# Optimization experiments

Hardware: AMD Instinct MI355X
Metric: run time of the kernel (lower is better)

## Reference

```python
import jax, jax.numpy as jnp
import numpy as np
import math

B, T, D, H, P, NPASS = 2, 2048, 1024, 16, 256, 3


def setup_inputs() -> dict:
    key = jax.random.key(0)
    ks = jax.random.split(key, 8)
    x = jax.random.normal(ks[0], (B, T, D), jnp.float32)
    scale_gamma = 1.0 + 0.1 * jax.random.normal(ks[1], (D,), jnp.float32)
    scale_beta = 0.1 * jax.random.normal(ks[2], (D,), jnp.float32)
    qkv_w = 0.02 * jax.random.normal(ks[3], (3 * D, D), jnp.float32)
    o_w = 0.02 * jax.random.normal(ks[4], (D, D), jnp.float32)
    norm1_w = jnp.ones((D,), jnp.float32)
    norm2_w = jnp.ones((D,), jnp.float32)
    angles = 0.1 * jax.random.normal(ks[5], (NPASS, P), jnp.float32)
    gate = jnp.ones((NPASS, D), jnp.float32)
    bias = jnp.zeros((NPASS, D), jnp.float32)
    # seeded random permutations matching torch.manual_seed(42+p*1000); torch.randperm
    pis, pjs = [], []
    for p in range(NPASS):
        rng = np.random.RandomState(42 + p * 1000)
        perm = rng.permutation(D)
        pis.append(perm[:P])
        pjs.append(perm[P:2 * P])
    pi = jnp.asarray(np.stack(pis), jnp.int32)
    pj = jnp.asarray(np.stack(pjs), jnp.int32)
    return dict(x=x, scale_gamma=scale_gamma, scale_beta=scale_beta, qkv_w=qkv_w,
                o_w=o_w, norm1_w=norm1_w, norm2_w=norm2_w, angles=angles,
                gate=gate, bias=bias, pi=pi, pj=pj)


def _rmsnorm(x, w):
    eps = jnp.finfo(x.dtype).eps
    return x * jax.lax.rsqrt(jnp.mean(x * x, axis=-1, keepdims=True) + eps) * w


def reference(x, scale_gamma, scale_beta, qkv_w, o_w, norm1_w, norm2_w,
              angles, gate, bias, pi, pj):
    Bs, Ts, Ds = x.shape
    hd = Ds // H
    # --- attention branch ---
    h = _rmsnorm(x, norm1_w) * scale_gamma + scale_beta
    qkv = (h @ qkv_w.T).reshape(Bs, Ts, 3, H, hd)
    qkv = jnp.moveaxis(qkv, 2, 0)            # [3, B, T, H, hd]
    q, k, v = (jnp.swapaxes(qkv[i], 1, 2) for i in range(3))  # [B, H, T, hd]
    scores = jnp.einsum('bhqd,bhkd->bhqk', q, k) / math.sqrt(hd)
    causal = jnp.tril(jnp.ones((Ts, Ts), bool))
    scores = jnp.where(causal, scores, -jnp.inf)
    attn = jax.nn.softmax(scores, axis=-1)
    out = jnp.einsum('bhqk,bhkd->bhqd', attn, v)
    out = jnp.swapaxes(out, 1, 2).reshape(Bs, Ts, Ds)
    x = x + out @ o_w.T
    # --- rotation pseudo-FFN branch ---
    h = _rmsnorm(x, norm2_w) * scale_gamma + scale_beta
    r = h
    for p in range(NPASS):
        cos_a = jnp.cos(angles[p])
        sin_a = jnp.sin(angles[p])
        hi = r[..., pi[p]]
        hj = r[..., pj[p]]
        r = r.at[..., pi[p]].set(hi * cos_a - hj * sin_a)
        r = r.at[..., pj[p]].set(hi * sin_a + hj * cos_a)
        r = jax.nn.silu(r * gate[p] + bias[p])
    return x + r - h
```

## Files before the change

### kernel.cpp

```cpp
#include <hip/hip_runtime.h>
#include <hip/hip_bf16.h>

#define B_ 2
#define T_ 2048
#define D_ 1024
#define H_ 16
#define HD_ 64
#define NP_ 3
#define P_ 256

#define SCALE2 0.18033688011112042f

typedef short bf16x8 __attribute__((ext_vector_type(8)));
typedef float f32x4 __attribute__((ext_vector_type(4)));

__device__ __forceinline__ float bf2f(__hip_bfloat16 v) { return __bfloat162float(v); }
__device__ __forceinline__ __hip_bfloat16 f2bf(float v) { return __float2bfloat16(v); }

__device__ __forceinline__ unsigned pack2bf(float a, float b) {
    union { __hip_bfloat16 h; unsigned short u; } ua, ub;
    ua.h = f2bf(a); ub.h = f2bf(b);
    return (unsigned)ua.u | ((unsigned)ub.u << 16);
}

#define GLOAD_LDS16(gp, lp) \
    __builtin_amdgcn_global_load_lds( \
        (const __attribute__((address_space(1))) void*)(gp), \
        (__attribute__((address_space(3))) void*)(lp), 16, 0, 0)

__global__ __launch_bounds__(256) void detect_kernel(
    const unsigned short* __restrict__ xs, int* __restrict__ flag)
{
    __shared__ int cnt;
    if (threadIdx.x == 0) cnt = 0;
    __syncthreads();
    int bad = 0;
    for (int i = threadIdx.x; i < 16384; i += 256) {
        int e = (xs[i] >> 7) & 0xFF;
        if (e >= 0xB8) bad++;
    }
    if (bad) atomicAdd(&cnt, bad);
    __syncthreads();
    if (threadIdx.x == 0) *flag = (cnt >= 8) ? 1 : 0;
}

__global__ __launch_bounds__(256) void cvt16_2_kernel(
    const void* __restrict__ a, const void* __restrict__ bsrc,
    __hip_bfloat16* __restrict__ da, __hip_bfloat16* __restrict__ db,
    int na, int ntot, const int* __restrict__ flag)
{
    int i = blockIdx.x * 256 + threadIdx.x;
    if (i >= ntot) return;
    int f = *flag;
    if (i < na)
        da[i] = f ? f2bf(((const float*)a)[i]) : ((const __hip_bfloat16*)a)[i];
    else {
        int k = i - na;
        db[k] = f ? f2bf(((const float*)bsrc)[k]) : ((const __hip_bfloat16*)bsrc)[k];
    }
}

__global__ __launch_bounds__(256) void cvt_small_kernel(
    const void* __restrict__ g,  const void* __restrict__ b,
    const void* __restrict__ n1, const void* __restrict__ n2,
    const void* __restrict__ ang, const void* __restrict__ gt,
    const void* __restrict__ bi,
    float* __restrict__ dst, const int* __restrict__ flag)
{
    int i = blockIdx.x * 256 + threadIdx.x;
    if (i >= 11008) return;
    const void* src; int off;
    if      (i < 1024) { src = g;   off = i; }
    else if (i < 2048) { src = b;   off = i - 1024; }
    else if (i < 3072) { src = n1;  off = i - 2048; }
    else if (i < 4096) { src = n2;  off = i - 3072; }
    else if (i < 4864) { src = ang; off = i - 4096; }
    else if (i < 7936) { src = gt;  off = i - 4864; }
    else               { src = bi;  off = i - 7936; }
    dst[i] = (*flag) ? ((const float*)src)[off]
                     : bf2f(((const __hip_bfloat16*)src)[off]);
}

__global__ __launch_bounds__(256) void rmsnorm1_kernel(
    const void* __restrict__ xraw,
    const float* __restrict__ gamma,
    const float* __restrict__ beta,
    const float* __restrict__ w,
    const int* __restrict__ flag,
    __hip_bfloat16* __restrict__ out)
{
    int row = blockIdx.x;
    int t = threadIdx.x;
    int f = *flag;
    float eps = f ? 1.1920929e-7f : 0.0078125f;
    float v[4];
    if (f) {
        const float4 xv = ((const float4*)((const float*)xraw + (size_t)row * D_))[t];
        v[0] = xv.x; v[1] = xv.y; v[2] = xv.z; v[3] = xv.w;
    } else {
        const __hip_bfloat16* xr = (const __hip_bfloat16*)xraw + (size_t)row * D_;
#pragma unroll
        for (int c = 0; c < 4; c++) v[c] = bf2f(xr[t * 4 + c]);
    }
    float ss = 0.f;
#pragma unroll
    for (int c = 0; c < 4; c++) ss += v[c] * v[c];
#pragma unroll
    for (int m = 32; m; m >>= 1) ss += __shfl_xor(ss, m, 64);
    __shared__ float red[4];
    int wv = t >> 6;
    if ((t & 63) == 0) red[wv] = ss;
    __syncthreads();
    float scale = rsqrtf((red[0] + red[1] + red[2] + red[3]) * (1.0f / D_) + eps);
#pragma unroll
    for (int c = 0; c < 4; c++) {
        int e = t * 4 + c;
        size_t idx = (size_t)row * D_ + e;
        out[idx] = f2bf(v[c] * scale * w[e] * gamma[e] + beta[e]);
    }
}

__global__ __launch_bounds__(256) void gemm_bt_bf16_kernel(
    const __hip_bfloat16* __restrict__ A,
    const __hip_bfloat16* __restrict__ Bm,
    __hip_bfloat16* __restrict__ C,
    int M, int N, int K, int nscale, float qscale)
{
    __shared__ __attribute__((aligned(16))) __hip_bfloat16 As[128 * 32];
    __shared__ __attribute__((aligned(16))) __hip_bfloat16 Bs[128 * 32];
    int tid = threadIdx.x;
    int bm = blockIdx.y, bn = blockIdx.x;
    int lane = tid & 63, wv = tid >> 6;
    int wm = wv >> 1, wn = wv & 1;
    int q = lane >> 4, mr = lane & 15;

    f32x4 acc[4][4] = {};

    for (int k0 = 0; k0 < K; k0 += 32) {
#pragma unroll
        for (int s = 0; s < 2; s++) {
            int e = (s * 256 + tid) * 8;
            int r = e >> 5, c = e & 31;
            GLOAD_LDS16(&A[(size_t)(bm * 128 + r) * K + k0 + c], &As[e]);
            GLOAD_LDS16(&Bm[(size_t)(bn * 128 + r) * K + k0 + c], &Bs[e]);
        }
        __syncthreads();
        bf16x8 af[4], bfr[4];
#pragma unroll
        for (int i = 0; i < 4; i++)
            af[i] = *(const bf16x8*)(&As[(wm * 64 + i * 16 + mr) * 32 + q * 8]);
#pragma unroll
        for (int j = 0; j < 4; j++)
            bfr[j] = *(const bf16x8*)(&Bs[(wn * 64 + j * 16 + mr) * 32 + q * 8]);
#pragma unroll
        for (int i = 0; i < 4; i++)
#pragma unroll
            for (int j = 0; j < 4; j++)
                acc[i][j] = __builtin_amdgcn_mfma_f32_16x16x32_bf16(af[i], bfr[j], acc[i][j], 0, 0, 0);
        __syncthreads();
    }

#pragma unroll
    for (int i = 0; i < 4; i++)
#pragma unroll
        for (int r = 0; r < 4; r++) {
            int m = bm * 128 + wm * 64 + i * 16 + q * 4 + r;
#pragma unroll
            for (int j = 0; j < 4; j++) {
                int n = bn * 128 + wn * 64 + j * 16 + mr;
                float vv = acc[i][j][r];
                if (n < nscale) vv *= qscale;
                C[(size_t)m * N + n] = f2bf(vv);
            }
        }
}

__global__ __launch_bounds__(256) void gemm_bt_resid_kernel(
    const __hip_bfloat16* __restrict__ A,
    const __hip_bfloat16* __restrict__ Bm,
    const void* __restrict__ xraw,
    const int* __restrict__ flag,
    float* __restrict__ C,
    int M, int N, int K)
{
    __shared__ __attribute__((aligned(16))) __hip_bfloat16 As[128 * 32];
    __shared__ __attribute__((aligned(16))) __hip_bfloat16 Bs[128 * 32];
    int tid = threadIdx.x;
    int bm = blockIdx.y, bn = blockIdx.x;
    int lane = tid & 63, wv = tid >> 6;
    int wm = wv >> 1, wn = wv & 1;
    int q = lane >> 4, mr = lane & 15;
    int f = *flag;

    f32x4 acc[4][4] = {};

    for (int k0 = 0; k0 < K; k0 += 32) {
#pragma unroll
        for (int s = 0; s < 2; s++) {
            int e = (s * 256 + tid) * 8;
            int r = e >> 5, c = e & 31;
            GLOAD_LDS16(&A[(size_t)(bm * 128 + r) * K + k0 + c], &As[e]);
            GLOAD_LDS16(&Bm[(size_t)(bn * 128 + r) * K + k0 + c], &Bs[e]);
        }
        __syncthreads();
        bf16x8 af[4], bfr[4];
#pragma unroll
        for (int i = 0; i < 4; i++)
            af[i] = *(const bf16x8*)(&As[(wm * 64 + i * 16 + mr) * 32 + q * 8]);
#pragma unroll
        for (int j = 0; j < 4; j++)
            bfr[j] = *(const bf16x8*)(&Bs[(wn * 64 + j * 16 + mr) * 32 + q * 8]);
#pragma unroll
        for (int i = 0; i < 4; i++)
#pragma unroll
            for (int j = 0; j < 4; j++)
                acc[i][j] = __builtin_amdgcn_mfma_f32_16x16x32_bf16(af[i], bfr[j], acc[i][j], 0, 0, 0);
        __syncthreads();
    }

#pragma unroll
    for (int i = 0; i < 4; i++)
#pragma unroll
        for (int r = 0; r < 4; r++) {
            int m = bm * 128 + wm * 64 + i * 16 + q * 4 + r;
#pragma unroll
            for (int j = 0; j < 4; j++) {
                int n = bn * 128 + wn * 64 + j * 16 + mr;
                size_t idx = (size_t)m * N + n;
                float rv = f ? ((const float*)xraw)[idx]
                             : bf2f(((const __hip_bfloat16*)xraw)[idx]);
                C[idx] = rv + acc[i][j][r];
            }
        }
}

__global__ __launch_bounds__(256, 4) void attn_kernel(
    const __hip_bfloat16* __restrict__ qkv,
    __hip_bfloat16* __restrict__ attn_out)
{
    __shared__ __attribute__((aligned(16))) __hip_bfloat16 Ks[2][64 * 64];
    __shared__ __attribute__((aligned(16))) __hip_bfloat16 Vts[2][64 * 64];
    __shared__ __attribute__((aligned(16))) unsigned int Pd[4 * 512];

    int id = blockIdx.x;
    int half = (id ^ (id >> 8)) & 1;
    int w4 = (id >> 1) & 15;
    int qt = half ? 31 - w4 : w4;
    int bh = (id >> 5) & 31;
    int b = bh >> 4, h = bh & 15;
    int tid = threadIdx.x, lane = tid & 63, wv = tid >> 6;
    int q = lane >> 4, mr = lane & 15;
    int m8 = mr & 7;

    const size_t rs3 = 3 * D_;
    const __hip_bfloat16* qp = qkv + (size_t)(b * T_) * rs3 + h * HD_;
    const __hip_bfloat16* kp = qp + D_;
    const __hip_bfloat16* vp = qp + 2 * D_;

    int sr = tid >> 2;
    int sc = (tid & 3) * 16;
    int lc0 = sc >> 3;
    int swk = sr & 7;
    int kk_ = (tid & 31) * 2;
    int dd = (tid >> 5) * 8;
    int vlc = kk_ >> 3, voff = kk_ & 7;

    bf16x8 aq0, aq1;
    {
        const __hip_bfloat16* qrow = qp + (size_t)(qt * 64 + wv * 16 + mr) * rs3;
        aq0 = *(const bf16x8*)(qrow + q * 8);
        aq1 = *(const bf16x8*)(qrow + 32 + q * 8);
    }

    bf16x8 kr0 = *(const bf16x8*)(kp + (size_t)sr * rs3 + sc);
    bf16x8 kr1 = *(const bf16x8*)(kp + (size_t)sr * rs3 + sc + 8);
    bf16x8 vr0 = *(const bf16x8*)(vp + (size_t)kk_ * rs3 + dd);
    bf16x8 vr1 = *(const bf16x8*)(vp + (size_t)(kk_ + 1) * rs3 + dd);
    *(bf16x8*)(&Ks[0][sr * 64 + ((lc0 ^ swk) * 8)]) = kr0;
    *(bf16x8*)(&Ks[0][sr * 64 + (((lc0 + 1) ^ swk) * 8)]) = kr1;
    {
        unsigned int* vd = (unsigned int*)&Vts[0][0];
#pragma unroll
        for (int i = 0; i < 8; i++) {
            unsigned int wd = ((unsigned int)(unsigned short)vr0[i]) |
                              (((unsigned int)(unsigned short)vr1[i]) << 16);
            vd[((dd + i) * 64 + ((vlc ^ i) * 8 + voff)) >> 1] = wd;
        }
    }
    __syncthreads();

    float l_run = 0.f;
    f32x4 o_acc[4] = {};
    unsigned int* Pw = &Pd[wv * 512];
    int qloc = wv * 16 + mr;

    for (int s = 0; s <= qt; s++) {
        int buf = s & 1;

        if (s < qt) {
            int ktn = s + 1;
            kr0 = *(const bf16x8*)(kp + (size_t)(ktn * 64 + sr) * rs3 + sc);
            kr1 = *(const bf16x8*)(kp + (size_t)(ktn * 64 + sr) * rs3 + sc + 8);
            vr0 = *(const bf16x8*)(vp + (size_t)(ktn * 64 + kk_) * rs3 + dd);
            vr1 = *(const bf16x8*)(vp + (size_t)(ktn * 64 + kk_ + 1) * rs3 + dd);
        }

        f32x4 sv[4] = {};
        {
            const __hip_bfloat16* Kb = &Ks[buf][0];
#pragma unroll
            for (int jn = 0; jn < 4; jn++)
                sv[jn] = __builtin_amdgcn_mfma_f32_16x16x32_bf16(
                    *(const bf16x8*)(&Kb[(jn * 16 + mr) * 64 + ((q ^ m8) * 8)]),
                    aq0, sv[jn], 0, 0, 0);
#pragma unroll
            for (int jn = 0; jn < 4; jn++)
                sv[jn] = __builtin_amdgcn_mfma_f32_16x16x32_bf16(
                    *(const bf16x8*)(&Kb[(jn * 16 + mr) * 64 + (((4 + q) ^ m8) * 8)]),
                    aq1, sv[jn], 0, 0, 0);
        }

        if (s == qt) {
#pragma unroll
            for (int jn = 0; jn < 4; jn++)
#pragma unroll
                for (int r = 0; r < 4; r++)
                    if (jn * 16 + q * 4 + r > qloc) sv[jn][r] = -1e30f;
        }

        float psum = 0.f;
#pragma unroll
        for (int jn = 0; jn < 4; jn++)
#pragma unroll
            for (int r = 0; r < 4; r++) {
                float p = exp2f(sv[jn][r]);
                sv[jn][r] = p;
                psum += p;
            }
        psum += __shfl_xor(psum, 16, 64);
        psum += __shfl_xor(psum, 32, 64);
        l_run += psum;

#pragma unroll
        for (int jn = 0; jn < 4; jn++) {
            uint2 val;
            val.x = pack2bf(sv[jn][0], sv[jn][1]);
            val.y = pack2bf(sv[jn][2], sv[jn][3]);
            int dw4 = 2 * jn + (q >> 1);
            *(uint2*)(&Pw[mr * 32 + ((dw4 ^ m8) << 2) + 2 * (q & 1)]) = val;
        }

#pragma unroll
        for (int kk = 0; kk < 2; kk++) {
            bf16x8 bp = *(const bf16x8*)(&Pw[mr * 32 + (((4 * kk + q) ^ m8) << 2)]);
#pragma unroll
            for (int dt = 0; dt < 4; dt++) {
                bf16x8 bv = *(const bf16x8*)(&Vts[buf][(dt * 16 + mr) * 64 + (((kk * 4 + q) ^ m8) * 8)]);
                o_acc[dt] = __builtin_amdgcn_mfma_f32_16x16x32_bf16(bv, bp, o_acc[dt], 0, 0, 0);
            }
        }

        if (s < qt) {
            *(bf16x8*)(&Ks[buf ^ 1][sr * 64 + ((lc0 ^ swk) * 8)]) = kr0;
            *(bf16x8*)(&Ks[buf ^ 1][sr * 64 + (((lc0 + 1) ^ swk) * 8)]) = kr1;
            unsigned int* vd = (unsigned int*)&Vts[buf ^ 1][0];
#pragma unroll
            for (int i = 0; i < 8; i++) {
                unsigned int wd = ((unsigned int)(unsigned short)vr0[i]) |
                                  (((unsigned int)(unsigned short)vr1[i]) << 16);
                vd[((dd + i) * 64 + ((vlc ^ i) * 8 + voff)) >> 1] = wd;
            }
        }
        __syncthreads();
    }

    {
        float inv = 1.0f / l_run;
        int trow = qt * 64 + wv * 16 + mr;
        __hip_bfloat16* op = attn_out + (size_t)(b * T_ + trow) * D_ + h * HD_;
#pragma unroll
        for (int dt = 0; dt < 4; dt++) {
            uint2 val;
            val.x = pack2bf(o_acc[dt][0] * inv, o_acc[dt][1] * inv);
            val.y = pack2bf(o_acc[dt][2] * inv, o_acc[dt][3] * inv);
            *(uint2*)(op + dt * 16 + q * 4) = val;
        }
    }
}

__global__ __launch_bounds__(256) void final_kernel(
    const float* __restrict__ xn,
    const float* __restrict__ gamma,
    const float* __restrict__ beta,
    const float* __restrict__ w2,
    const float* __restrict__ angles,
    const float* __restrict__ gate,
    const float* __restrict__ bias,
    const int* __restrict__ pi,
    const int* __restrict__ pj,
    const int* __restrict__ flag,
    void* __restrict__ outp)
{
    __shared__ float rbuf[D_];
    __shared__ float red[4];
    int row = blockIdx.x, t = threadIdx.x;
    int f = *flag;
    float eps = f ? 1.1920929e-7f : 0.0078125f;
    const float* xr = xn + (size_t)row * D_;
    float x4[4];
    float ss = 0.f;
#pragma unroll
    for (int c = 0; c < 4; c++) { x4[c] = xr[t * 4 + c]; ss += x4[c] * x4[c]; }
#pragma unroll
    for (int m = 32; m; m >>= 1) ss += __shfl_xor(ss, m, 64);
    int wv = t >> 6;
    if ((t & 63) == 0) red[wv] = ss;
    __syncthreads();
    float scale = rsqrtf((red[0] + red[1] + red[2] + red[3]) * (1.0f / D_) + eps);
    float hloc[4];
#pragma unroll
    for (int c = 0; c < 4; c++) {
        int e = t * 4 + c;
        float hv = x4[c] * scale * w2[e] * gamma[e] + beta[e];
        hloc[c] = hv;
        rbuf[e] = hv;
    }
    __syncthreads();
    for (int p = 0; p < NP_; p++) {
        float a = angles[p * P_ + t];
        float ca = __cosf(a), sa = __sinf(a);
        int ip = pi[p * P_ + t], jp = pj[p * P_ + t];
        float hi = rbuf[ip], hj = rbuf[jp];
        rbuf[ip] = hi * ca - hj * sa;
        rbuf[jp] = hi * sa + hj * ca;
        __syncthreads();
#pragma unroll
        for (int c = 0; c < 4; c++) {
            int e = t * 4 + c;
            float v = rbuf[e] * gate[p * D_ + e] + bias[p * D_ + e];
            rbuf[e] = v / (1.f + __expf(-v));
        }
        __syncthreads();
    }
#pragma unroll
    for (int c = 0; c < 4; c++) {
        int e = t * 4 + c;
        float ov = x4[c] + rbuf[e] - hloc[c];
        size_t idx = (size_t)row * D_ + e;
        if (f) ((float*)outp)[idx] = ov;
        else   ((__hip_bfloat16*)outp)[idx] = f2bf(ov);
    }
}

extern "C" void kernel_launch(void* const* d_in, const int* in_sizes, int n_in,
                              void* d_out, int out_size, void* d_ws, size_t ws_size,
                              hipStream_t stream)
{
    const void* x      = d_in[0];
    const void* gamma  = d_in[1];
    const void* beta   = d_in[2];
    const void* qkv_w  = d_in[3];
    const void* o_w    = d_in[4];
    const void* n1w    = d_in[5];
    const void* n2w    = d_in[6];
    const void* angles = d_in[7];
    const void* gate   = d_in[8];
    const void* bias   = d_in[9];
    const int* pi = (const int*)d_in[10];
    const int* pj = (const int*)d_in[11];

    const int M = B_ * T_;
    char* ws = (char*)d_ws;
    const size_t MB = 1u << 20;
    int*   flag   = (int*)ws;
    float* smalls = (float*)(ws + 4096);
    float* gf   = smalls;
    float* bf   = smalls + 1024;
    float* n1f  = smalls + 2048;
    float* n2f  = smalls + 3072;
    float* angf = smalls + 4096;
    float* gtf  = smalls + 4864;
    float* bif  = smalls + 7936;
    __hip_bfloat16* wbf  = (__hip_bfloat16*)(ws + 17 * MB);
    __hip_bfloat16* owbf = (__hip_bfloat16*)(ws + 23 * MB);
    __hip_bfloat16* h1   = (__hip_bfloat16*)(ws + 25 * MB);
    __hip_bfloat16* qkv  = (__hip_bfloat16*)(ws + 33 * MB);
    float*          xnew = (float*)         (ws + 33 * MB);

    detect_kernel<<<1, 256, 0, stream>>>((const unsigned short*)x, flag);

    cvt_small_kernel<<<43, 256, 0, stream>>>(gamma, beta, n1w, n2w, angles, gate, bias,
                                             smalls, flag);
    cvt16_2_kernel<<<(4 * D_ * D_ + 255) / 256, 256, 0, stream>>>(
        qkv_w, o_w, wbf, owbf, 3 * D_ * D_, 4 * D_ * D_, flag);

    rmsnorm1_kernel<<<M, 256, 0, stream>>>(x, gf, bf, n1f, flag, h1);

    gemm_bt_bf16_kernel<<<dim3(3 * D_ / 128, M / 128), 256, 0, stream>>>(
        h1, wbf, qkv, M, 3 * D_, D_, D_, SCALE2);

    attn_kernel<<<dim3(1024), 256, 0, stream>>>(qkv, h1);

    gemm_bt_resid_kernel<<<dim3(D_ / 128, M / 128), 256, 0, stream>>>(
        h1, owbf, x, flag, xnew, M, D_, D_);

    final_kernel<<<M, 256, 0, stream>>>(xnew, gf, bf, n2f, angf, gtf, bif,
                                        pi, pj, flag, d_out);
}
```

Measured before the change: 249.0 us.

## Vectorize conversions and stores, use packed bf16 cvt, defer softmax row-sum reduction

Several small changes are bundled. The weight-conversion kernel now handles 8 elements per thread with vector loads and stores, and bf16 packing uses the v_cvt_pk_bf16_f32 instruction. The rmsnorm and final kernels use vector loads and packed stores. The attention kernel builds the V transpose words with byte permutes and moves the softmax row-sum shuffle reduction out of the key loop to a single reduction at the end. These target memory instruction count and per-iteration ALU work. The risk is that the inline asm rounding may differ slightly from __float2bfloat16.

```diff
diff --git a/kernel.cpp b/kernel.cpp
--- a/kernel.cpp
+++ b/kernel.cpp
@@ -18,9 +18,12 @@
 __device__ __forceinline__ __hip_bfloat16 f2bf(float v) { return __float2bfloat16(v); }
 
 __device__ __forceinline__ unsigned pack2bf(float a, float b) {
-    union { __hip_bfloat16 h; unsigned short u; } ua, ub;
-    ua.h = f2bf(a); ub.h = f2bf(b);
-    return (unsigned)ua.u | ((unsigned)ub.u << 16);
+    unsigned r;
+    asm("v_cvt_pk_bf16_f32 %0, %1, %2" : "=v"(r) : "v"(a), "v"(b));
+    return r;
+}
+__device__ __forceinline__ unsigned short f2bf_u(float v) {
+    return (unsigned short)pack2bf(v, v);
 }
 
 #define GLOAD_LDS16(gp, lp) \
@@ -49,14 +52,23 @@
     __hip_bfloat16* __restrict__ da, __hip_bfloat16* __restrict__ db,
     int na, int ntot, const int* __restrict__ flag)
 {
-    int i = blockIdx.x * 256 + threadIdx.x;
-    if (i >= ntot) return;
+    int i8 = (blockIdx.x * 256 + threadIdx.x) * 8;
+    if (i8 >= ntot) return;
     int f = *flag;
-    if (i < na)
-        da[i] = f ? f2bf(((const float*)a)[i]) : ((const __hip_bfloat16*)a)[i];
-    else {
-        int k = i - na;
-        db[k] = f ? f2bf(((const float*)bsrc)[k]) : ((const __hip_bfloat16*)bsrc)[k];
+    const void* src; __hip_bfloat16* dst; int off;
+    if (i8 < na) { src = a; dst = da; off = i8; }
+    else         { src = bsrc; dst = db; off = i8 - na; }
+    if (f) {
+        const float4* sp = (const float4*)((const float*)src + off);
+        float4 v0 = sp[0], v1 = sp[1];
+        uint4 o;
+        o.x = pack2bf(v0.x, v0.y);
+        o.y = pack2bf(v0.z, v0.w);
+        o.z = pack2bf(v1.x, v1.y);
+        o.w = pack2bf(v1.z, v1.w);
+        *(uint4*)(dst + off) = o;
+    } else {
+        *(uint4*)(dst + off) = *(const uint4*)((const __hip_bfloat16*)src + off);
     }
 }
 
@@ -98,9 +110,11 @@
         const float4 xv = ((const float4*)((const float*)xraw + (size_t)row * D_))[t];
         v[0] = xv.x; v[1] = xv.y; v[2] = xv.z; v[3] = xv.w;
     } else {
-        const __hip_bfloat16* xr = (const __hip_bfloat16*)xraw + (size_t)row * D_;
-#pragma unroll
-        for (int c = 0; c < 4; c++) v[c] = bf2f(xr[t * 4 + c]);
+        const uint2 u = ((const uint2*)((const __hip_bfloat16*)xraw + (size_t)row * D_))[t];
+        v[0] = __uint_as_float(u.x << 16);
+        v[1] = __uint_as_float(u.x & 0xffff0000u);
+        v[2] = __uint_as_float(u.y << 16);
+        v[3] = __uint_as_float(u.y & 0xffff0000u);
     }
     float ss = 0.f;
 #pragma unroll
@@ -112,12 +126,16 @@
     if ((t & 63) == 0) red[wv] = ss;
     __syncthreads();
     float scale = rsqrtf((red[0] + red[1] + red[2] + red[3]) * (1.0f / D_) + eps);
+    float o[4];
 #pragma unroll
     for (int c = 0; c < 4; c++) {
         int e = t * 4 + c;
-        size_t idx = (size_t)row * D_ + e;
-        out[idx] = f2bf(v[c] * scale * w[e] * gamma[e] + beta[e]);
-    }
+        o[c] = v[c] * scale * w[e] * gamma[e] + beta[e];
+    }
+    uint2 pkd;
+    pkd.x = pack2bf(o[0], o[1]);
+    pkd.y = pack2bf(o[2], o[3]);
+    *(uint2*)(out + (size_t)row * D_ + t * 4) = pkd;
 }
 
 __global__ __launch_bounds__(256) void gemm_bt_bf16_kernel(
@@ -170,7 +188,7 @@
                 int n = bn * 128 + wn * 64 + j * 16 + mr;
                 float vv = acc[i][j][r];
                 if (n < nscale) vv *= qscale;
-                C[(size_t)m * N + n] = f2bf(vv);
+                ((unsigned short*)C)[(size_t)m * N + n] = f2bf_u(vv);
             }
         }
 }
@@ -280,16 +298,20 @@
     *(bf16x8*)(&Ks[0][sr * 64 + (((lc0 + 1) ^ swk) * 8)]) = kr1;
     {
         unsigned int* vd = (unsigned int*)&Vts[0][0];
-#pragma unroll
-        for (int i = 0; i < 8; i++) {
-            unsigned int wd = ((unsigned int)(unsigned short)vr0[i]) |
-                              (((unsigned int)(unsigned short)vr1[i]) << 16);
-            vd[((dd + i) * 64 + ((vlc ^ i) * 8 + voff)) >> 1] = wd;
+        union { bf16x8 v; unsigned u[4]; } ua, ub;
+        ua.v = vr0; ub.v = vr1;
+#pragma unroll
+        for (int w = 0; w < 4; w++) {
+            unsigned lo = __builtin_amdgcn_perm(ub.u[w], ua.u[w], 0x05040100u);
+            unsigned hi = __builtin_amdgcn_perm(ub.u[w], ua.u[w], 0x07060302u);
+            int i0 = 2 * w, i1 = 2 * w + 1;
+            vd[((dd + i0) * 64 + ((vlc ^ i0) * 8 + voff)) >> 1] = lo;
+            vd[((dd + i1) * 64 + ((vlc ^ i1) * 8 + voff)) >> 1] = hi;
         }
     }
     __syncthreads();
 
-    float l_run = 0.f;
+    float l_part = 0.f;
     f32x4 o_acc[4] = {};
     unsigned int* Pw = &Pd[wv * 512];
     int qloc = wv * 16 + mr;
@@ -328,18 +350,14 @@
                     if (jn * 16 + q * 4 + r > qloc) sv[jn][r] = -1e30f;
         }
 
-        float psum = 0.f;
 #pragma unroll
         for (int jn = 0; jn < 4; jn++)
 #pragma unroll
             for (int r = 0; r < 4; r++) {
                 float p = exp2f(sv[jn][r]);
                 sv[jn][r] = p;
-                psum += p;
+                l_part += p;
             }
-        psum += __shfl_xor(psum, 16, 64);
-        psum += __shfl_xor(psum, 32, 64);
-        l_run += psum;
 
 #pragma unroll
         for (int jn = 0; jn < 4; jn++) {
@@ -364,15 +382,23 @@
             *(bf16x8*)(&Ks[buf ^ 1][sr * 64 + ((lc0 ^ swk) * 8)]) = kr0;
             *(bf16x8*)(&Ks[buf ^ 1][sr * 64 + (((lc0 + 1) ^ swk) * 8)]) = kr1;
             unsigned int* vd = (unsigned int*)&Vts[buf ^ 1][0];
-#pragma unroll
-            for (int i = 0; i < 8; i++) {
-                unsigned int wd = ((unsigned int)(unsigned short)vr0[i]) |
-                                  (((unsigned int)(unsigned short)vr1[i]) << 16);
-                vd[((dd + i) * 64 + ((vlc ^ i) * 8 + voff)) >> 1] = wd;
+            union { bf16x8 v; unsigned u[4]; } ua, ub;
+            ua.v = vr0; ub.v = vr1;
+#pragma unroll
+            for (int w = 0; w < 4; w++) {
+                unsigned lo = __builtin_amdgcn_perm(ub.u[w], ua.u[w], 0x05040100u);
+                unsigned hi = __builtin_amdgcn_perm(ub.u[w], ua.u[w], 0x07060302u);
+                int i0 = 2 * w, i1 = 2 * w + 1;
+                vd[((dd + i0) * 64 + ((vlc ^ i0) * 8 + voff)) >> 1] = lo;
+                vd[((dd + i1) * 64 + ((vlc ^ i1) * 8 + voff)) >> 1] = hi;
             }
         }
         __syncthreads();
     }
+
+    float l_run = l_part;
+    l_run += __shfl_xor(l_run, 16, 64);
+    l_run += __shfl_xor(l_run, 32, 64);
 
     {
         float inv = 1.0f / l_run;
@@ -406,11 +432,11 @@
     int row = blockIdx.x, t = threadIdx.x;
     int f = *flag;
     float eps = f ? 1.1920929e-7f : 0.0078125f;
-    const float* xr = xn + (size_t)row * D_;
-    float x4[4];
+    const float4 xv = ((const float4*)(xn + (size_t)row * D_))[t];
+    float x4[4] = {xv.x, xv.y, xv.z, xv.w};
     float ss = 0.f;
 #pragma unroll
-    for (int c = 0; c < 4; c++) { x4[c] = xr[t * 4 + c]; ss += x4[c] * x4[c]; }
+    for (int c = 0; c < 4; c++) ss += x4[c] * x4[c];
 #pragma unroll
     for (int m = 32; m; m >>= 1) ss += __shfl_xor(ss, m, 64);
     int wv = t >> 6;
@@ -491,7 +517,7 @@
 
     cvt_small_kernel<<<43, 256, 0, stream>>>(gamma, beta, n1w, n2w, angles, gate, bias,
                                              smalls, flag);
-    cvt16_2_kernel<<<(4 * D_ * D_ + 255) / 256, 256, 0, stream>>>(
+    cvt16_2_kernel<<<(4 * D_ * D_ / 8 + 255) / 256, 256, 0, stream>>>(
         qkv_w, o_w, wbf, owbf, 3 * D_ * D_, 4 * D_ * D_, flag);
 
     rmsnorm1_kernel<<<M, 256, 0, stream>>>(x, gf, bf, n1f, flag, h1);
```

New measurement: 245.1 us. No clear change (-1.6%).
